# Kernel tuning notes

Hardware: AMD Instinct MI355X
Metric: run time of the kernel (lower is better)

Reference implementation:

```python
import jax, jax.numpy as jnp
import numpy as np

B = 1048576
H = 32
DAMP_MIN = jnp.array([0.001, 0.001], dtype=jnp.float32)

def setup_inputs() -> dict:
    key = jax.random.key(0)
    ks = jax.random.split(key, 13)
    u = lambda k, shape: jax.random.uniform(k, shape, jnp.float32, -0.2, 0.2)
    return {
        "x": jax.random.normal(ks[0], (B, 2), jnp.float32),
        "w_d1": u(ks[1], (2, H)),
        "w_d2": u(ks[2], (H, H)),
        "w_d3": u(ks[3], (H, 2)),
        "w_o1": u(ks[4], (2, H)),
        "w_o2": u(ks[5], (H, H)),
        "w_o3": u(ks[6], (H, 1)),
        "b_d1": jnp.zeros((H,), jnp.float32),
        "b_d2": jnp.zeros((H,), jnp.float32),
        "b_d3": jnp.zeros((2,), jnp.float32),
        "b_o1": jnp.zeros((H,), jnp.float32),
        "b_o2": jnp.zeros((H,), jnp.float32),
        "b_o3": jnp.zeros((1,), jnp.float32),
    }

def reference(x, w_d1, w_d2, w_d3, w_o1, w_o2, w_o3,
              b_d1, b_d2, b_d3, b_o1, b_o2, b_o3):
    # diag branch: 2-layer tanh MLP -> relu, scaled by x
    d1t = jnp.tanh(x @ w_d1 + b_d1)
    d2t = jnp.tanh(d1t @ w_d2 + b_d2)
    d3 = d2t @ w_d3 + b_d3                       # [B,2]
    d3r = (jax.nn.relu(d3) + DAMP_MIN) * x       # diag of L, [B,2]
    # off-diag branch -> single lower-triangular element per sample
    o1t = jnp.tanh(x @ w_o1 + b_o1)
    o2t = jnp.tanh(o1t @ w_o2 + b_o2)
    o3 = o2t @ w_o3 + b_o3                       # [B,1]
    # L = [[a,0],[c,b]] per sample; D = (L L^T) x, vectorized over batch.
    a = d3r[:, 0]
    b = d3r[:, 1]
    c = o3[:, 0]
    x0 = x[:, 0]
    x1 = x[:, 1]
    D0 = a * a * x0 + a * c * x1
    D1 = a * c * x0 + (c * c + b * b) * x1
    return jnp.stack([D0, D1], axis=-1)          # [B,2]
```

## Files before the change

### kernel.cpp

```cpp
#include <hip/hip_runtime.h>


typedef __bf16 bf16x8 __attribute__((ext_vector_type(8)));
typedef float f32x4 __attribute__((ext_vector_type(4)));
typedef int i32x4 __attribute__((ext_vector_type(4)));

__device__ __forceinline__ float fast_tanh(float x) {
    float e = __builtin_amdgcn_exp2f(x * 2.8853900817779268f);
    float r = __builtin_amdgcn_rcpf(e + 1.0f);
    return __builtin_fmaf(-2.0f, r, 1.0f);
}

__device__ __forceinline__ int pack_bf16(float f0, float f1) {
    unsigned u0 = __builtin_bit_cast(unsigned, f0) + 0x8000u;
    unsigned u1 = __builtin_bit_cast(unsigned, f1) + 0x8000u;
    return (int)__builtin_amdgcn_perm(u1, u0, 0x07060302u);
}

__global__ __launch_bounds__(256, 3) void damping_mfma(
    const float* __restrict__ x,
    const float* __restrict__ w_d1, const float* __restrict__ w_d2, const float* __restrict__ w_d3,
    const float* __restrict__ w_o1, const float* __restrict__ w_o2, const float* __restrict__ w_o3,
    const float* __restrict__ b_d1, const float* __restrict__ b_d2, const float* __restrict__ b_d3,
    const float* __restrict__ b_o1, const float* __restrict__ b_o2, const float* __restrict__ b_o3,
    float* __restrict__ out, int n_tiles)
{
    const int lane = threadIdx.x & 63;
    const int quad = lane >> 4;
    const int b16  = lane & 15;
    const int wid     = (int)((blockIdx.x * blockDim.x + threadIdx.x) >> 6);
    const int n_waves = (int)((gridDim.x * blockDim.x) >> 6);

    float w1d0[8], w1d1[8], bd1[8], w1o0[8], w1o1[8], bo1[8];
    #pragma unroll
    for (int j = 0; j < 8; ++j) {
        int k = quad * 8 + j;
        w1d0[j] = w_d1[k]; w1d1[j] = w_d1[32 + k]; bd1[j] = b_d1[k];
        w1o0[j] = w_o1[k]; w1o1[j] = w_o1[32 + k]; bo1[j] = b_o1[k];
    }
    bf16x8 a_d2[2], a_o2[2];
    #pragma unroll
    for (int t = 0; t < 2; ++t) {
        #pragma unroll
        for (int j = 0; j < 8; ++j) {
            int k = quad * 8 + j;
            a_d2[t][j] = (__bf16)w_d2[k * 32 + t * 16 + b16];
            a_o2[t][j] = (__bf16)w_o2[k * 32 + t * 16 + b16];
        }
    }
    float bd2[8], bo2[8], w3d0[8], w3d1[8], w3o[8];
    #pragma unroll
    for (int i = 0; i < 8; ++i) {
        int jj = (i >> 2) * 16 + quad * 4 + (i & 3);
        bd2[i]  = b_d2[jj]; bo2[i] = b_o2[jj];
        w3d0[i] = w_d3[jj * 2]; w3d1[i] = w_d3[jj * 2 + 1];
        w3o[i]  = w_o3[jj];
    }
    const float bd3_0 = b_d3[0], bd3_1 = b_d3[1], bo3_0 = b_o3[0];

    const float2* x2 = (const float2*)x;
    int tile = wid;
    if (tile >= n_tiles) return;
    float2 xv = x2[tile * 16 + b16];

    for (; tile < n_tiles; tile += n_waves) {
        int nt = tile + n_waves;
        nt = (nt < n_tiles) ? nt : tile;
        float2 xnext = x2[nt * 16 + b16];

        const float x0 = xv.x, x1 = xv.y;

        float hd[8], ho[8];
        #pragma unroll
        for (int j = 0; j < 8; ++j) {
            hd[j] = fast_tanh(fmaf(x1, w1d1[j], fmaf(x0, w1d0[j], bd1[j])));
            ho[j] = fast_tanh(fmaf(x1, w1o1[j], fmaf(x0, w1o0[j], bo1[j])));
        }
        i32x4 pd_, po_;
        #pragma unroll
        for (int p = 0; p < 4; ++p) {
            pd_[p] = pack_bf16(hd[2 * p], hd[2 * p + 1]);
            po_[p] = pack_bf16(ho[2 * p], ho[2 * p + 1]);
        }
        bf16x8 bfd = __builtin_bit_cast(bf16x8, pd_);
        bf16x8 bfo = __builtin_bit_cast(bf16x8, po_);

        f32x4 zero = {0.f, 0.f, 0.f, 0.f};
        f32x4 d0 = __builtin_amdgcn_mfma_f32_16x16x32_bf16(a_d2[0], bfd, zero, 0, 0, 0);
        f32x4 d1 = __builtin_amdgcn_mfma_f32_16x16x32_bf16(a_d2[1], bfd, zero, 0, 0, 0);
        f32x4 o0 = __builtin_amdgcn_mfma_f32_16x16x32_bf16(a_o2[0], bfo, zero, 0, 0, 0);
        f32x4 o1 = __builtin_amdgcn_mfma_f32_16x16x32_bf16(a_o2[1], bfo, zero, 0, 0, 0);

        float pd0 = 0.f, pd1 = 0.f, po = 0.f;
        #pragma unroll
        for (int i = 0; i < 8; ++i) {
            float vd = (i < 4 ? d0[i] : d1[i - 4]) + bd2[i];
            float vo = (i < 4 ? o0[i] : o1[i - 4]) + bo2[i];
            float h2d = fast_tanh(vd);
            float h2o = fast_tanh(vo);
            pd0 = fmaf(h2d, w3d0[i], pd0);
            pd1 = fmaf(h2d, w3d1[i], pd1);
            po  = fmaf(h2o, w3o[i], po);
        }
        pd0 += __shfl_xor(pd0, 16); pd0 += __shfl_xor(pd0, 32);
        pd1 += __shfl_xor(pd1, 16); pd1 += __shfl_xor(pd1, 32);
        po  += __shfl_xor(po, 16);  po  += __shfl_xor(po, 32);

        float d30 = pd0 + bd3_0, d31 = pd1 + bd3_1, c = po + bo3_0;
        float a = (fmaxf(d30, 0.f) + 0.001f) * x0;
        float b = (fmaxf(d31, 0.f) + 0.001f) * x1;
        float D0 = fmaf(a * a, x0, a * c * x1);
        float D1 = fmaf(a * c, x0, fmaf(c, c, b * b) * x1);

        if (quad == 0) ((float2*)out)[tile * 16 + b16] = make_float2(D0, D1);
        xv = xnext;
    }
}

extern "C" void kernel_launch(void* const* d_in, const int* in_sizes, int n_in,
                              void* d_out, int out_size, void* d_ws, size_t ws_size,
                              hipStream_t stream) {
    const float* x    = (const float*)d_in[0];
    const float* w_d1 = (const float*)d_in[1];
    const float* w_d2 = (const float*)d_in[2];
    const float* w_d3 = (const float*)d_in[3];
    const float* w_o1 = (const float*)d_in[4];
    const float* w_o2 = (const float*)d_in[5];
    const float* w_o3 = (const float*)d_in[6];
    const float* b_d1 = (const float*)d_in[7];
    const float* b_d2 = (const float*)d_in[8];
    const float* b_d3 = (const float*)d_in[9];
    const float* b_o1 = (const float*)d_in[10];
    const float* b_o2 = (const float*)d_in[11];
    const float* b_o3 = (const float*)d_in[12];
    float* out = (float*)d_out;

    int n = in_sizes[0] / 2;
    int n_tiles = n / 16;
    int blocks_needed = (n_tiles + 3) / 4;
    int grid = blocks_needed < 768 ? blocks_needed : 768;
    damping_mfma<<<grid, 256, 0, stream>>>(
        x, w_d1, w_d2, w_d3, w_o1, w_o2, w_o3,
        b_d1, b_d2, b_d3, b_o1, b_o2, b_o3, out, n_tiles);
}
```

Measured before the change: 127.4 us.

## Fold tanh scale into weights, drop x prefetch, raise occupancy and grid

Pre-multiplies the layer-1 and layer-2 weights and biases by the tanh exp2 scale, which removes one multiply per tanh evaluation. Removes the software prefetch of the next tile's x, lowering register pressure, and raises the launch-bounds occupancy hint from 3 to 7 blocks along with a larger grid (1792 blocks). The aim is to hide memory latency through more resident waves rather than explicit prefetch. Scaling the layer-2 weights before the bf16 cast slightly changes the rounding.

```diff
diff --git a/kernel.cpp b/kernel.cpp
--- a/kernel.cpp
+++ b/kernel.cpp
@@ -5,8 +5,10 @@
 typedef float f32x4 __attribute__((ext_vector_type(4)));
 typedef int i32x4 __attribute__((ext_vector_type(4)));
 
-__device__ __forceinline__ float fast_tanh(float x) {
-    float e = __builtin_amdgcn_exp2f(x * 2.8853900817779268f);
+#define TANH_SCALE 2.8853900817779268f
+
+__device__ __forceinline__ float fast_tanh_pre(float y) {
+    float e = __builtin_amdgcn_exp2f(y);
     float r = __builtin_amdgcn_rcpf(e + 1.0f);
     return __builtin_fmaf(-2.0f, r, 1.0f);
 }
@@ -17,7 +19,7 @@
     return (int)__builtin_amdgcn_perm(u1, u0, 0x07060302u);
 }
 
-__global__ __launch_bounds__(256, 3) void damping_mfma(
+__global__ __launch_bounds__(256, 7) void damping_mfma(
     const float* __restrict__ x,
     const float* __restrict__ w_d1, const float* __restrict__ w_d2, const float* __restrict__ w_d3,
     const float* __restrict__ w_o1, const float* __restrict__ w_o2, const float* __restrict__ w_o3,
@@ -35,8 +37,10 @@
     #pragma unroll
     for (int j = 0; j < 8; ++j) {
         int k = quad * 8 + j;
-        w1d0[j] = w_d1[k]; w1d1[j] = w_d1[32 + k]; bd1[j] = b_d1[k];
-        w1o0[j] = w_o1[k]; w1o1[j] = w_o1[32 + k]; bo1[j] = b_o1[k];
+        w1d0[j] = w_d1[k] * TANH_SCALE; w1d1[j] = w_d1[32 + k] * TANH_SCALE;
+        bd1[j]  = b_d1[k] * TANH_SCALE;
+        w1o0[j] = w_o1[k] * TANH_SCALE; w1o1[j] = w_o1[32 + k] * TANH_SCALE;
+        bo1[j]  = b_o1[k] * TANH_SCALE;
     }
     bf16x8 a_d2[2], a_o2[2];
     #pragma unroll
@@ -44,37 +48,31 @@
         #pragma unroll
         for (int j = 0; j < 8; ++j) {
             int k = quad * 8 + j;
-            a_d2[t][j] = (__bf16)w_d2[k * 32 + t * 16 + b16];
-            a_o2[t][j] = (__bf16)w_o2[k * 32 + t * 16 + b16];
+            a_d2[t][j] = (__bf16)(w_d2[k * 32 + t * 16 + b16] * TANH_SCALE);
+            a_o2[t][j] = (__bf16)(w_o2[k * 32 + t * 16 + b16] * TANH_SCALE);
         }
     }
     float bd2[8], bo2[8], w3d0[8], w3d1[8], w3o[8];
     #pragma unroll
     for (int i = 0; i < 8; ++i) {
         int jj = (i >> 2) * 16 + quad * 4 + (i & 3);
-        bd2[i]  = b_d2[jj]; bo2[i] = b_o2[jj];
+        bd2[i]  = b_d2[jj] * TANH_SCALE; bo2[i] = b_o2[jj] * TANH_SCALE;
         w3d0[i] = w_d3[jj * 2]; w3d1[i] = w_d3[jj * 2 + 1];
         w3o[i]  = w_o3[jj];
     }
     const float bd3_0 = b_d3[0], bd3_1 = b_d3[1], bo3_0 = b_o3[0];
 
     const float2* x2 = (const float2*)x;
-    int tile = wid;
-    if (tile >= n_tiles) return;
-    float2 xv = x2[tile * 16 + b16];
 
-    for (; tile < n_tiles; tile += n_waves) {
-        int nt = tile + n_waves;
-        nt = (nt < n_tiles) ? nt : tile;
-        float2 xnext = x2[nt * 16 + b16];
-
+    for (int tile = wid; tile < n_tiles; tile += n_waves) {
+        float2 xv = x2[tile * 16 + b16];
         const float x0 = xv.x, x1 = xv.y;
 
         float hd[8], ho[8];
         #pragma unroll
         for (int j = 0; j < 8; ++j) {
-            hd[j] = fast_tanh(fmaf(x1, w1d1[j], fmaf(x0, w1d0[j], bd1[j])));
-            ho[j] = fast_tanh(fmaf(x1, w1o1[j], fmaf(x0, w1o0[j], bo1[j])));
+            hd[j] = fast_tanh_pre(fmaf(x1, w1d1[j], fmaf(x0, w1d0[j], bd1[j])));
+            ho[j] = fast_tanh_pre(fmaf(x1, w1o1[j], fmaf(x0, w1o0[j], bo1[j])));
         }
         i32x4 pd_, po_;
         #pragma unroll
@@ -96,8 +94,8 @@
         for (int i = 0; i < 8; ++i) {
             float vd = (i < 4 ? d0[i] : d1[i - 4]) + bd2[i];
             float vo = (i < 4 ? o0[i] : o1[i - 4]) + bo2[i];
-            float h2d = fast_tanh(vd);
-            float h2o = fast_tanh(vo);
+            float h2d = fast_tanh_pre(vd);
+            float h2o = fast_tanh_pre(vo);
             pd0 = fmaf(h2d, w3d0[i], pd0);
             pd1 = fmaf(h2d, w3d1[i], pd1);
             po  = fmaf(h2o, w3o[i], po);
@@ -113,7 +111,6 @@
         float D1 = fmaf(a * c, x0, fmaf(c, c, b * b) * x1);
 
         if (quad == 0) ((float2*)out)[tile * 16 + b16] = make_float2(D0, D1);
-        xv = xnext;
     }
 }
 
@@ -138,7 +135,7 @@
     int n = in_sizes[0] / 2;
     int n_tiles = n / 16;
     int blocks_needed = (n_tiles + 3) / 4;
-    int grid = blocks_needed < 768 ? blocks_needed : 768;
+    int grid = blocks_needed < 1792 ? blocks_needed : 1792;
     damping_mfma<<<grid, 256, 0, stream>>>(
         x, w_d1, w_d2, w_d3, w_o1, w_o2, w_o3,
         b_d1, b_d2, b_d3, b_o1, b_o2, b_o3, out, n_tiles);
```

Result: slower. 249.0 us (+95.4%).
